# Performance work log

Hardware: AMD Instinct MI355X
Metric: run time of the kernel (lower is better)

Reference implementation:

```python
import jax, jax.numpy as jnp
import numpy as np

C, H_HEADS, L_LEV, M_PTS = 256, 4, 3, 4
TAU0 = 1.0


def _ln(x, g, b, eps=1e-5):
    mu = x.mean(-1, keepdims=True)
    var = ((x - mu) ** 2).mean(-1, keepdims=True)
    return (x - mu) * jax.lax.rsqrt(var + eps) * g + b


def _grid_sample(v, grid):
    """Bilinear grid_sample, padding_mode='zeros', align_corners=True.
    v: [B,C,Hin,Win], grid: [B,N,2] (x,y) in [-1,1] -> [B,N,C]"""
    B, Cc, Hin, Win = v.shape
    x = (grid[..., 0] + 1.0) * 0.5 * (Win - 1)
    y = (grid[..., 1] + 1.0) * 0.5 * (Hin - 1)
    x0 = jnp.floor(x); y0 = jnp.floor(y)
    wx1 = x - x0; wy1 = y - y0
    x0i = x0.astype(jnp.int32); y0i = y0.astype(jnp.int32)
    vflat = v.reshape(B, Cc, Hin * Win).transpose(0, 2, 1)  # [B,HW,C]

    def tap(yi, xi, w):
        valid = ((xi >= 0) & (xi < Win) & (yi >= 0) & (yi < Hin)).astype(v.dtype)
        idx = jnp.clip(yi, 0, Hin - 1) * Win + jnp.clip(xi, 0, Win - 1)  # [B,N]
        g = jax.vmap(lambda vf, i: vf[i])(vflat, idx)  # [B,N,C]
        return g * (w * valid)[..., None]

    return (tap(y0i, x0i, (1 - wy1) * (1 - wx1))
            + tap(y0i, x0i + 1, (1 - wy1) * wx1)
            + tap(y0i + 1, x0i, wy1 * (1 - wx1))
            + tap(y0i + 1, x0i + 1, wy1 * wx1))


def setup_inputs() -> dict:
    key = jax.random.key(0)
    ks = jax.random.split(key, 32)
    B, Hq, Wq = 2, 64, 64
    cins = [256, 512, 1024]
    d = {
        'S':  jax.random.normal(ks[0], (B, C, Hq, Wq), jnp.float32),
        'f0': jax.random.normal(ks[1], (B, cins[0], 64, 64), jnp.float32),
        'f1': jax.random.normal(ks[2], (B, cins[1], 32, 32), jnp.float32),
        'f2': jax.random.normal(ks[3], (B, cins[2], 16, 16), jnp.float32),
        'sim': jax.random.uniform(ks[4], (B, 1, Hq, Wq), jnp.float32),
        # 1x1 conv value projections per level
        'vw0': jax.random.normal(ks[5], (C, cins[0]), jnp.float32) * 0.02,
        'vb0': jnp.zeros((C,), jnp.float32),
        'vw1': jax.random.normal(ks[6], (C, cins[1]), jnp.float32) * 0.02,
        'vb1': jnp.zeros((C,), jnp.float32),
        'vw2': jax.random.normal(ks[7], (C, cins[2]), jnp.float32) * 0.02,
        'vb2': jnp.zeros((C,), jnp.float32),
        'q_w': jax.random.normal(ks[8], (C, C), jnp.float32) * 0.02,
        'q_b': jnp.zeros((C,), jnp.float32),
        # offset/weight predictors (non-zero so sampling is nontrivial)
        'off_w': jax.random.normal(ks[9], (H_HEADS * L_LEV * M_PTS * 2, C), jnp.float32) * 0.01,
        'off_b': jnp.zeros((H_HEADS * L_LEV * M_PTS * 2,), jnp.float32),
        'wgt_w': jax.random.normal(ks[10], (H_HEADS * L_LEV * M_PTS, C), jnp.float32) * 0.02,
        'wgt_b': jnp.zeros((H_HEADS * L_LEV * M_PTS,), jnp.float32),
        'out_w': jax.random.normal(ks[11], (C, H_HEADS * C), jnp.float32) * 0.02,
        'out_b': jnp.zeros((C,), jnp.float32),
        'lnq_g': jnp.ones((C,), jnp.float32), 'lnq_b': jnp.zeros((C,), jnp.float32),
        'lno_g': jnp.ones((C,), jnp.float32), 'lno_b': jnp.zeros((C,), jnp.float32),
        'fc1_w': jax.random.normal(ks[12], (4 * C, C), jnp.float32) * 0.02,
        'fc1_b': jnp.zeros((4 * C,), jnp.float32),
        'fc2_w': jax.random.normal(ks[13], (C, 4 * C), jnp.float32) * 0.02,
        'fc2_b': jnp.zeros((C,), jnp.float32),
    }
    return d


def reference(S, f0, f1, f2, sim, vw0, vb0, vw1, vb1, vw2, vb2, q_w, q_b,
              off_w, off_b, wgt_w, wgt_b, out_w, out_b,
              lnq_g, lnq_b, lno_g, lno_b, fc1_w, fc1_b, fc2_w, fc2_b):
    B, Cc, Hq, Wq = S.shape
    Nq = Hq * Wq
    S_seq = S.reshape(B, Cc, Nq).transpose(0, 2, 1)  # [B,Nq,C]
    Q = _ln(S_seq @ q_w.T + q_b, lnq_g, lnq_b)

    # reference points in [0,1], (x,y)
    ys = jnp.linspace(0.5 / Hq, 1 - 0.5 / Hq, Hq)
    xs = jnp.linspace(0.5 / Wq, 1 - 0.5 / Wq, Wq)
    yy, xx = jnp.meshgrid(ys, xs, indexing='ij')
    ref = jnp.stack([xx, yy], axis=-1).reshape(1, Nq, 2)

    feats = [(f0, vw0, vb0), (f1, vw1, vb1), (f2, vw2, vb2)]
    V = [jnp.einsum('bchw,oc->bohw', f, w) + b[None, :, None, None] for f, w, b in feats]

    off = (Q @ off_w.T + off_b).reshape(B, Nq, H_HEADS, L_LEV, M_PTS, 2)
    wts = (Q @ wgt_w.T + wgt_b).reshape(B, Nq, H_HEADS, L_LEV, M_PTS)

    sim2 = sim[:, 0].reshape(B, Nq, 1)
    tau = TAU0 / (sim2 + 0.001)
    wts = wts / tau.reshape(B, Nq, 1, 1, 1)
    wts = jax.nn.softmax(wts.reshape(B, Nq, H_HEADS, L_LEV * M_PTS), axis=-1)
    wts = wts.reshape(B, Nq, H_HEADS, L_LEV, M_PTS)

    acc = jnp.zeros((B, Nq, H_HEADS, Cc), S.dtype)
    for l in range(L_LEV):
        g01 = ref.reshape(1, Nq, 1, 1, 2) + off[:, :, :, l]  # [B,Nq,H,M,2]
        g = jnp.clip(jnp.tanh(g01 * 2.0 - 1.0), -1.0, 1.0)
        samp = _grid_sample(V[l], g.reshape(B, Nq * H_HEADS * M_PTS, 2))
        samp = samp.reshape(B, Nq, H_HEADS, M_PTS, Cc)
        acc = acc + jnp.einsum('bqhmc,bqhm->bqhc', samp, wts[:, :, :, l])

    Y = acc.reshape(B, Nq, H_HEADS * Cc) @ out_w.T + out_b
    Z = _ln(S_seq + Y, lno_g, lno_b)
    h = jax.nn.gelu(Z @ fc1_w.T + fc1_b, approximate=False)
    Z = Z + (h @ fc2_w.T + fc2_b)
    return Z.transpose(0, 2, 1).reshape(B, Cc, Hq, Wq)
```

## Files before the change

### kernel.cpp

```cpp
#include <hip/hip_runtime.h>
#include <hip/hip_bf16.h>
#include <math.h>

#define NQ 4096
#define CC 256

typedef __attribute__((ext_vector_type(8))) short bfrag;
typedef __attribute__((ext_vector_type(4))) float ffrag;

__device__ inline unsigned short f2bf(float x) {
  __hip_bfloat16 h = __float2bfloat16(x);
  return *reinterpret_cast<unsigned short*>(&h);
}

__device__ inline void gload16(const void* g, void* l) {
  __builtin_amdgcn_global_load_lds(
      (const __attribute__((address_space(1))) void*)g,
      (__attribute__((address_space(3))) void*)l, 16, 0, 0);
}

__device__ void tr64(const float* __restrict__ src,
                     unsigned short* __restrict__ dstb, int Cin, int P,
                     int p0, int c0, int b, float (*t)[73]) {
  int tid = threadIdx.x;
  int rx = tid & 15, ry = tid >> 4;
  const float* Sb = src + (size_t)b * Cin * P + p0 + rx * 4;
  #pragma unroll
  for (int i = 0; i < 4; i++) {
    int r = ry + i * 16;
    float4 v = *(const float4*)(Sb + (size_t)(c0 + r) * P);
    t[r][rx * 4 + 0] = v.x; t[r][rx * 4 + 1] = v.y;
    t[r][rx * 4 + 2] = v.z; t[r][rx * 4 + 3] = v.w;
  }
  __syncthreads();
  size_t ob = (size_t)b * P * Cin;
  #pragma unroll
  for (int i = 0; i < 4; i++) {
    int pr = ry + i * 16;
    float x0 = t[rx * 4 + 0][pr], x1 = t[rx * 4 + 1][pr];
    float x2 = t[rx * 4 + 2][pr], x3 = t[rx * 4 + 3][pr];
    size_t idx = ob + (size_t)(p0 + pr) * Cin + c0 + rx * 4;
    ushort4 u4;
    u4.x = f2bf(x0); u4.y = f2bf(x1); u4.z = f2bf(x2); u4.w = f2bf(x3);
    *(ushort4*)(dstb + idx) = u4;
  }
}

__global__ __launch_bounds__(256)
void prep_all_k(const float* S, const float* f0, const float* f1, const float* f2,
                const float* q_w, const float* off_w, const float* wgt_w,
                const float* vw0, const float* vw1, const float* vw2,
                const float* out_w, const float* fc1_w, const float* fc2_w,
                const float* off_b, const float* wgt_b,
                unsigned short* Sbf,
                unsigned short* Xf0, unsigned short* Xf1, unsigned short* Xf2,
                unsigned short* q_wb, unsigned short* owb,
                unsigned short* vw0b, unsigned short* vw1b, unsigned short* vw2b,
                unsigned short* out_wb, unsigned short* fc1_wb,
                unsigned short* fc2_wb, float* bias144) {
  __shared__ float t[64][73];
  int bid = blockIdx.x;
  if (bid < 512) {
    int l = bid;
    tr64(S, Sbf, 256, 4096, (l & 63) * 64, ((l >> 6) & 3) * 64, l >> 8, t);
  } else if (bid < 1024) {
    int l = bid - 512;
    tr64(f0, Xf0, 256, 4096, (l & 63) * 64, ((l >> 6) & 3) * 64, l >> 8, t);
  } else if (bid < 1280) {
    int l = bid - 1024;
    tr64(f1, Xf1, 512, 1024, (l & 15) * 64, ((l >> 4) & 7) * 64, l >> 7, t);
  } else if (bid < 1408) {
    int l = bid - 1280;
    tr64(f2, Xf2, 1024, 256, (l & 3) * 64, ((l >> 2) & 15) * 64, l >> 6, t);
  } else if (bid < 2688) {
    int i4 = (bid - 1408) * 256 + threadIdx.x;
    const float* src; unsigned short* dst;
    if (i4 < 16384)       { src = q_w;   dst = q_wb; }
    else if (i4 < 32768)  { i4 -= 16384;  src = vw0;   dst = vw0b; }
    else if (i4 < 65536)  { i4 -= 32768;  src = vw1;   dst = vw1b; }
    else if (i4 < 131072) { i4 -= 65536;  src = vw2;   dst = vw2b; }
    else if (i4 < 196608) { i4 -= 131072; src = out_w; dst = out_wb; }
    else if (i4 < 262144) { i4 -= 196608; src = fc1_w; dst = fc1_wb; }
    else                  { i4 -= 262144; src = fc2_w; dst = fc2_wb; }
    float4 v = ((const float4*)src)[i4];
    ushort4 u; u.x = f2bf(v.x); u.y = f2bf(v.y); u.z = f2bf(v.z); u.w = f2bf(v.w);
    ((ushort4*)dst)[i4] = u;
  } else {
    int e = (bid - 2688) * 256 + threadIdx.x;
    float v = (e < 24576) ? off_w[e] : (e < 36864 ? wgt_w[e - 24576] : 0.f);
    owb[e] = f2bf(v);
    if (e < 96) bias144[e] = off_b[e];
    else if (e < 144) bias144[e] = wgt_b[e - 96];
  }
}

template<int BM, int BN, int WM, int WN, int EPI>
__device__ __forceinline__ void gemm_body(
    const unsigned short* __restrict__ A, const unsigned short* __restrict__ B,
    const float* __restrict__ bias, float* __restrict__ outf,
    unsigned short* __restrict__ outb, int N, int K, int ldo,
    const float* __restrict__ Zres, float* __restrict__ outT,
    int m0, int n0, unsigned short* As, unsigned short* Bs) {
  constexpr int MI = BM / (WM * 16), NI = BN / (WN * 16);
  constexpr int TA = BM / 8, TB = BN / 8;
  constexpr int LBM = (BM == 32) ? 5 : (BM == 64) ? 6 : 7;
  constexpr int LBN = (BN == 64) ? 6 : (BN == 128) ? 7 : 8;
  int tid = threadIdx.x, wave = tid >> 6, lane = tid & 63;
  int quad = lane >> 4, l16 = lane & 15;
  int wm = wave / WN, wn = wave % WN;
  const int mbase = wm * (BM / WM), nbase = wn * (BN / WN);

  ffrag acc[MI][NI];
  #pragma unroll
  for (int i = 0; i < MI; i++)
    #pragma unroll
    for (int j = 0; j < NI; j++) acc[i][j] = (ffrag)0.f;

  for (int k0 = 0; k0 < K; k0 += 64) {
    __syncthreads();
    for (int t = wave; t < TA + TB; t += 4) {
      if (t < TA) {
        int s = t * 64 + lane;
        int kc = s >> LBM, r = s & (BM - 1);
        gload16(A + (size_t)(m0 + r) * K + k0 + kc * 8, (char*)As + t * 1024);
      } else {
        int s = (t - TA) * 64 + lane;
        int kc = s >> LBN, r = s & (BN - 1);
        gload16(B + (size_t)(n0 + r) * K + k0 + kc * 8, (char*)Bs + (t - TA) * 1024);
      }
    }
    __syncthreads();
    #pragma unroll
    for (int ks = 0; ks < 2; ks++) {
      bfrag af[MI], bf[NI];
      #pragma unroll
      for (int mi = 0; mi < MI; mi++)
        af[mi] = *(const bfrag*)(As + ((((ks * 4 + quad) << LBM) + mbase + mi * 16 + l16) << 3));
      #pragma unroll
      for (int ni = 0; ni < NI; ni++)
        bf[ni] = *(const bfrag*)(Bs + ((((ks * 4 + quad) << LBN) + nbase + ni * 16 + l16) << 3));
      #pragma unroll
      for (int mi = 0; mi < MI; mi++)
        #pragma unroll
        for (int ni = 0; ni < NI; ni++)
          acc[mi][ni] = __builtin_amdgcn_mfma_f32_16x16x32_bf16(
              af[mi], bf[ni], acc[mi][ni], 0, 0, 0);
    }
  }

  if (EPI == 2) {
    #pragma unroll
    for (int mi = 0; mi < MI; mi++) {
      int mrow = m0 + mbase + mi * 16 + quad * 4;
      int bb = mrow >> 12, q0 = mrow & (NQ - 1);
      #pragma unroll
      for (int ni = 0; ni < NI; ni++) {
        int n = n0 + nbase + ni * 16 + l16;
        float bv = bias[n];
        float4 v;
        v.x = acc[mi][ni][0] + bv + Zres[(size_t)(mrow + 0) * CC + n];
        v.y = acc[mi][ni][1] + bv + Zres[(size_t)(mrow + 1) * CC + n];
        v.z = acc[mi][ni][2] + bv + Zres[(size_t)(mrow + 2) * CC + n];
        v.w = acc[mi][ni][3] + bv + Zres[(size_t)(mrow + 3) * CC + n];
        *(float4*)(outT + ((size_t)(bb * CC + n)) * NQ + q0) = v;
      }
    }
  } else {
    #pragma unroll
    for (int mi = 0; mi < MI; mi++) {
      int mrow = m0 + mbase + mi * 16 + quad * 4;
      #pragma unroll
      for (int ni = 0; ni < NI; ni++) {
        int n = n0 + nbase + ni * 16 + l16;
        if (n < N) {
          float bv = bias[n];
          #pragma unroll
          for (int r = 0; r < 4; r++) {
            float v = acc[mi][ni][r] + bv;
            if (EPI == 1) {
              v = 0.5f * v * (1.f + erff(v * 0.70710678118654752f));
              outb[(size_t)(mrow + r) * ldo + n] = f2bf(v);
            } else if (EPI == 3) {
              outb[(size_t)(mrow + r) * ldo + n] = f2bf(v);
            } else {
              outf[(size_t)(mrow + r) * ldo + n] = v;
            }
          }
        }
      }
    }
  }
}

template<bool RES>
__device__ __forceinline__ void gemm_ln_body(
    const unsigned short* __restrict__ A, const unsigned short* __restrict__ B,
    const float* __restrict__ bias, const float* __restrict__ Sraw,
    float* __restrict__ outf, unsigned short* __restrict__ outb,
    const float* __restrict__ g, const float* __restrict__ be,
    int K, int m0, char* sm) {
  unsigned short* As = (unsigned short*)sm;
  unsigned short* Bs = (unsigned short*)(sm + 4096);
  float* L = (float*)sm;

  int tid = threadIdx.x, wave = tid >> 6, lane = tid & 63;
  int quad = lane >> 4, l16 = lane & 15;

  ffrag acc[2][4];
  #pragma unroll
  for (int i = 0; i < 2; i++)
    #pragma unroll
    for (int j = 0; j < 4; j++) acc[i][j] = (ffrag)0.f;

  for (int k0 = 0; k0 < K; k0 += 64) {
    __syncthreads();
    for (int t = wave; t < 36; t += 4) {
      if (t < 4) {
        int s = t * 64 + lane;
        int kc = s >> 5, r = s & 31;
        gload16(A + (size_t)(m0 + r) * K + k0 + kc * 8, sm + t * 1024);
      } else {
        int s = (t - 4) * 64 + lane;
        int kc = s >> 8, r = s & 255;
        gload16(B + (size_t)r * K + k0 + kc * 8, sm + 4096 + (t - 4) * 1024);
      }
    }
    __syncthreads();
    #pragma unroll
    for (int ks = 0; ks < 2; ks++) {
      bfrag af[2], bf[4];
      #pragma unroll
      for (int mi = 0; mi < 2; mi++)
        af[mi] = *(const bfrag*)(As + ((((ks * 4 + quad) << 5) + mi * 16 + l16) << 3));
      #pragma unroll
      for (int ni = 0; ni < 4; ni++)
        bf[ni] = *(const bfrag*)(Bs + ((((ks * 4 + quad) << 8) + wave * 64 + ni * 16 + l16) << 3));
      #pragma unroll
      for (int mi = 0; mi < 2; mi++)
        #pragma unroll
        for (int ni = 0; ni < 4; ni++)
          acc[mi][ni] = __builtin_amdgcn_mfma_f32_16x16x32_bf16(
              af[mi], bf[ni], acc[mi][ni], 0, 0, 0);
    }
  }
  __syncthreads();

  #pragma unroll
  for (int mi = 0; mi < 2; mi++) {
    int row = mi * 16 + quad * 4;
    int m = m0 + row;
    int bb = m >> 12, q0 = m & (NQ - 1);
    #pragma unroll
    for (int ni = 0; ni < 4; ni++) {
      int col = wave * 64 + ni * 16 + l16;
      float bv = bias[col];
      float4 s4 = make_float4(0.f, 0.f, 0.f, 0.f);
      if (RES) s4 = *(const float4*)(Sraw + ((size_t)(bb * CC + col)) * NQ + q0);
      L[(row + 0) * 264 + col] = acc[mi][ni][0] + bv + s4.x;
      L[(row + 1) * 264 + col] = acc[mi][ni][1] + bv + s4.y;
      L[(row + 2) * 264 + col] = acc[mi][ni][2] + bv + s4.z;
      L[(row + 3) * 264 + col] = acc[mi][ni][3] + bv + s4.w;
    }
  }
  __syncthreads();

  int row = tid >> 3, j = tid & 7;
  int seg = ((j + row) & 7) * 32;
  const float* Lr = L + row * 264 + seg;
  float s1 = 0.f, s2 = 0.f;
  #pragma unroll
  for (int i = 0; i < 8; i++) {
    float4 t4 = *(const float4*)(Lr + i * 4);
    s1 += t4.x + t4.y + t4.z + t4.w;
    s2 += t4.x * t4.x + t4.y * t4.y + t4.z * t4.z + t4.w * t4.w;
  }
  #pragma unroll
  for (int o = 1; o < 8; o <<= 1) {
    s1 += __shfl_xor(s1, o);
    s2 += __shfl_xor(s2, o);
  }
  float mu = s1 * (1.f / 256.f);
  float var = s2 * (1.f / 256.f) - mu * mu;
  float rs = rsqrtf(var + 1e-5f);
  int gm = m0 + row;
  #pragma unroll
  for (int i = 0; i < 8; i++) {
    int col = seg + i * 4;
    float4 t4 = *(const float4*)(Lr + i * 4);
    float4 gg = *(const float4*)(g + col);
    float4 bb4 = *(const float4*)(be + col);
    float4 y;
    y.x = (t4.x - mu) * rs * gg.x + bb4.x;
    y.y = (t4.y - mu) * rs * gg.y + bb4.y;
    y.z = (t4.z - mu) * rs * gg.z + bb4.z;
    y.w = (t4.w - mu) * rs * gg.w + bb4.w;
    ushort4 ub;
    ub.x = f2bf(y.x); ub.y = f2bf(y.y); ub.z = f2bf(y.z); ub.w = f2bf(y.w);
    *(ushort4*)(outb + (size_t)gm * CC + col) = ub;
    if (RES) *(float4*)(outf + (size_t)gm * CC + col) = y;
  }
}

__global__ __launch_bounds__(256)
void qv_k(const unsigned short* Sbf, const unsigned short* q_wb, const float* q_b,
          const float* lnq_g, const float* lnq_b, unsigned short* Qbf,
          const unsigned short* Xf0, const unsigned short* Xf1,
          const unsigned short* Xf2, const unsigned short* vw0b,
          const unsigned short* vw1b, const unsigned short* vw2b,
          const float* vb0, const float* vb1, const float* vb2,
          unsigned short* V0b, unsigned short* V1b, unsigned short* V2b) {
  __shared__ __attribute__((aligned(16))) char sm[36864];
  int bid = blockIdx.x;
  if (bid < 256) {
    gemm_ln_body<false>(Sbf, q_wb, q_b, nullptr, nullptr, Qbf,
                        lnq_g, lnq_b, 256, bid * 32, sm);
  } else {
    int lb = bid - 256;
    const unsigned short *A, *B; const float* bias; unsigned short* out; int K;
    if (lb < 256)      { A = Xf0; B = vw0b; bias = vb0; out = V0b; K = 256; }
    else if (lb < 320) { A = Xf1; B = vw1b; bias = vb1; out = V1b; K = 512;  lb -= 256; }
    else               { A = Xf2; B = vw2b; bias = vb2; out = V2b; K = 1024; lb -= 320; }
    int n0 = (lb & 1) * 128, m0 = (lb >> 1) * 64;
    gemm_body<64, 128, 2, 2, 3>(A, B, bias, nullptr, out, 256, K, 256,
                                nullptr, nullptr, m0, n0,
                                (unsigned short*)sm, (unsigned short*)(sm + 8192));
  }
}

__global__ __launch_bounds__(256)
void outln_k(const unsigned short* accbf, const unsigned short* out_wb,
             const float* out_b, const float* S, float* Z,
             unsigned short* Zbf, const float* lno_g, const float* lno_b) {
  __shared__ __attribute__((aligned(16))) char sm[36864];
  gemm_ln_body<true>(accbf, out_wb, out_b, S, Z, Zbf,
                     lno_g, lno_b, 1024, blockIdx.x * 32, sm);
}

__global__ __launch_bounds__(256)
void offwgt_k(const unsigned short* Qbf, const unsigned short* owb,
              const float* bias144, float* offwgt) {
  __shared__ __attribute__((aligned(16))) unsigned short As[4096];
  __shared__ __attribute__((aligned(16))) unsigned short Bs[8192];
  gemm_body<64, 128, 2, 2, 0>(Qbf, owb, bias144, offwgt, nullptr, 144, 256, 144,
                              nullptr, nullptr, blockIdx.y * 64, blockIdx.x * 128, As, Bs);
}

__global__ __launch_bounds__(256)
void fc1_k(const unsigned short* Zbf, const unsigned short* fc1_wb,
           const float* fc1_b, unsigned short* hbf) {
  __shared__ __attribute__((aligned(16))) unsigned short As[8192];
  __shared__ __attribute__((aligned(16))) unsigned short Bs[8192];
  gemm_body<128, 128, 2, 2, 1>(Zbf, fc1_wb, fc1_b, nullptr, hbf, 1024, 256, 1024,
                               nullptr, nullptr, blockIdx.y * 128, blockIdx.x * 128, As, Bs);
}

__global__ __launch_bounds__(256)
void fc2_k(const unsigned short* hbf, const unsigned short* fc2_wb,
           const float* fc2_b, const float* Z, float* outp) {
  __shared__ __attribute__((aligned(16))) unsigned short As[4096];
  __shared__ __attribute__((aligned(16))) unsigned short Bs[4096];
  gemm_body<64, 64, 2, 2, 2>(hbf, fc2_wb, fc2_b, nullptr, nullptr, 256, 1024, 256,
                             Z, outp, blockIdx.y * 64, blockIdx.x * 64, As, Bs);
}

__global__ __launch_bounds__(256)
void sample_k(const float* __restrict__ ow, const float* __restrict__ sim,
              const unsigned short* __restrict__ V0, const unsigned short* __restrict__ V1,
              const unsigned short* __restrict__ V2, unsigned short* __restrict__ acc) {
  int bn = blockIdx.x;
  int q = ((bn & 7) << 10) | (bn >> 3);
  int b = q >> 12, n = q & (NQ - 1);
  int tid = threadIdx.x, head = tid >> 6, lane = tid & 63;
  int half = lane >> 5, l32 = lane & 31;

  __shared__ float s_w[48];
  __shared__ int   s_xy[48][2];
  __shared__ float s_f[48][2];
  __shared__ uint2 s_ow[192];

  if (tid < 48) {
    int hh = tid / 12, pt = tid % 12, l = pt >> 2, mm = pt & 3;
    int oidx = (hh * 3 + l) * 4 + mm;
    float offx = ow[(size_t)q * 144 + oidx * 2 + 0];
    float offy = ow[(size_t)q * 144 + oidx * 2 + 1];
    float refx = ((n & 63) + 0.5f) * (1.f / 64.f);
    float refy = ((n >> 6) + 0.5f) * (1.f / 64.f);
    float gx = tanhf((refx + offx) * 2.f - 1.f);
    float gy = tanhf((refy + offy) * 2.f - 1.f);
    gx = fminf(1.f, fmaxf(-1.f, gx));
    gy = fminf(1.f, fmaxf(-1.f, gy));
    int Wl = 64 >> l;
    float x = (gx + 1.f) * 0.5f * (float)(Wl - 1);
    float y = (gy + 1.f) * 0.5f * (float)(Wl - 1);
    float x0 = floorf(x), y0 = floorf(y);
    s_xy[tid][0] = (int)x0;
    s_xy[tid][1] = (int)y0;
    s_f[tid][0] = x - x0;
    s_f[tid][1] = y - y0;
    s_w[tid] = ow[(size_t)q * 144 + 96 + oidx] * (sim[q] + 0.001f);
  }
  __syncthreads();
  if (tid < 4) {
    float mx = -1e30f;
    #pragma unroll
    for (int i = 0; i < 12; i++) mx = fmaxf(mx, s_w[tid * 12 + i]);
    float e[12], ssum = 0.f;
    #pragma unroll
    for (int i = 0; i < 12; i++) { e[i] = expf(s_w[tid * 12 + i] - mx); ssum += e[i]; }
    float inv = 1.f / ssum;
    #pragma unroll
    for (int i = 0; i < 12; i++) s_w[tid * 12 + i] = e[i] * inv;
  }
  __syncthreads();
  if (tid < 192) {
    int s = tid >> 2, tap = tid & 3;
    int l = (s % 12) >> 2;
    int Wl = 64 >> l;
    int X = s_xy[s][0] + (tap & 1), Y = s_xy[s][1] + (tap >> 1);
    bool valid = (X >= 0 && X < Wl && Y >= 0 && Y < Wl);
    float wx = (tap & 1) ? s_f[s][0] : 1.f - s_f[s][0];
    float wy = (tap >> 1) ? s_f[s][1] : 1.f - s_f[s][1];
    float twt = valid ? s_w[s] * wx * wy : 0.f;
    int Xc = min(max(X, 0), Wl - 1), Yc = min(max(Y, 0), Wl - 1);
    s_ow[tid].x = (unsigned)((Yc * Wl + Xc) << 8);
    s_ow[tid].y = __float_as_uint(twt);
  }
  __syncthreads();

  const unsigned short* B0 = V0 + (size_t)b * 4096 * CC;
  const unsigned short* B1 = V1 + (size_t)b * 1024 * CC;
  const unsigned short* B2 = V2 + (size_t)b * 256 * CC;
  int ch8 = l32 * 8;
  float a0 = 0.f, a1 = 0.f, a2 = 0.f, a3 = 0.f;
  float a4 = 0.f, a5 = 0.f, a6 = 0.f, a7 = 0.f;
  #pragma unroll
  for (int it = 0; it < 24; it++) {
    const unsigned short* base = (it < 8) ? B0 : (it < 16) ? B1 : B2;
    uint2 owv = s_ow[head * 48 + it * 2 + half];
    float w = __uint_as_float(owv.y);
    const uint4 u = *(const uint4*)(base + owv.x + ch8);
    a0 = fmaf(w, __uint_as_float(u.x << 16), a0);
    a1 = fmaf(w, __uint_as_float(u.x & 0xffff0000u), a1);
    a2 = fmaf(w, __uint_as_float(u.y << 16), a2);
    a3 = fmaf(w, __uint_as_float(u.y & 0xffff0000u), a3);
    a4 = fmaf(w, __uint_as_float(u.z << 16), a4);
    a5 = fmaf(w, __uint_as_float(u.z & 0xffff0000u), a5);
    a6 = fmaf(w, __uint_as_float(u.w << 16), a6);
    a7 = fmaf(w, __uint_as_float(u.w & 0xffff0000u), a7);
  }
  a0 += __shfl_xor(a0, 32); a1 += __shfl_xor(a1, 32);
  a2 += __shfl_xor(a2, 32); a3 += __shfl_xor(a3, 32);
  a4 += __shfl_xor(a4, 32); a5 += __shfl_xor(a5, 32);
  a6 += __shfl_xor(a6, 32); a7 += __shfl_xor(a7, 32);
  if (half == 0) {
    uint4 r;
    r.x = (unsigned)f2bf(a0) | ((unsigned)f2bf(a1) << 16);
    r.y = (unsigned)f2bf(a2) | ((unsigned)f2bf(a3) << 16);
    r.z = (unsigned)f2bf(a4) | ((unsigned)f2bf(a5) << 16);
    r.w = (unsigned)f2bf(a6) | ((unsigned)f2bf(a7) << 16);
    *(uint4*)(acc + (size_t)q * 1024 + head * CC + ch8) = r;
  }
}

extern "C" void kernel_launch(void* const* d_in, const int* in_sizes, int n_in,
                              void* d_out, int out_size, void* d_ws, size_t ws_size,
                              hipStream_t stream) {
  const float* S     = (const float*)d_in[0];
  const float* f0    = (const float*)d_in[1];
  const float* f1    = (const float*)d_in[2];
  const float* f2    = (const float*)d_in[3];
  const float* sim   = (const float*)d_in[4];
  const float* vw0   = (const float*)d_in[5];
  const float* vb0   = (const float*)d_in[6];
  const float* vw1   = (const float*)d_in[7];
  const float* vb1   = (const float*)d_in[8];
  const float* vw2   = (const float*)d_in[9];
  const float* vb2   = (const float*)d_in[10];
  const float* q_w   = (const float*)d_in[11];
  const float* q_b   = (const float*)d_in[12];
  const float* off_w = (const float*)d_in[13];
  const float* off_b = (const float*)d_in[14];
  const float* wgt_w = (const float*)d_in[15];
  const float* wgt_b = (const float*)d_in[16];
  const float* out_w = (const float*)d_in[17];
  const float* out_b = (const float*)d_in[18];
  const float* lnq_g = (const float*)d_in[19];
  const float* lnq_b = (const float*)d_in[20];
  const float* lno_g = (const float*)d_in[21];
  const float* lno_b = (const float*)d_in[22];
  const float* fc1_w = (const float*)d_in[23];
  const float* fc1_b = (const float*)d_in[24];
  const float* fc2_w = (const float*)d_in[25];
  const float* fc2_b = (const float*)d_in[26];

  char* p = (char*)d_ws;
  float* Z      = (float*)p; p += 8388608;
  float* offwgt = (float*)p; p += 4718592;
  float* bias144 = (float*)p; p += 1024;
  unsigned short* Sbf   = (unsigned short*)p; p += 4194304;
  unsigned short* Qbf   = (unsigned short*)p; p += 4194304;
  unsigned short* accbf = (unsigned short*)p; p += 16777216;
  unsigned short* V0b   = (unsigned short*)p; p += 4194304;
  unsigned short* V1b   = (unsigned short*)p; p += 1048576;
  unsigned short* V2b   = (unsigned short*)p; p += 262144;
  unsigned short* q_wb   = (unsigned short*)p; p += 131072;
  unsigned short* owb    = (unsigned short*)p; p += 131072;
  unsigned short* vw0b   = (unsigned short*)p; p += 131072;
  unsigned short* vw1b   = (unsigned short*)p; p += 262144;
  unsigned short* vw2b   = (unsigned short*)p; p += 524288;
  unsigned short* out_wb = (unsigned short*)p; p += 524288;
  unsigned short* fc1_wb = (unsigned short*)p; p += 524288;
  unsigned short* fc2_wb = (unsigned short*)p; p += 524288;

  unsigned short* Xf0 = accbf;
  unsigned short* Xf1 = accbf + 2097152;
  unsigned short* Xf2 = accbf + 3145728;
  unsigned short* Zbf = Qbf;
  unsigned short* hbf = accbf;
  float* outp = (float*)d_out;

  prep_all_k<<<2944, 256, 0, stream>>>(S, f0, f1, f2, q_w, off_w, wgt_w,
      vw0, vw1, vw2, out_w, fc1_w, fc2_w, off_b, wgt_b,
      Sbf, Xf0, Xf1, Xf2, q_wb, owb, vw0b, vw1b, vw2b, out_wb,
      fc1_wb, fc2_wb, bias144);

  qv_k<<<592, 256, 0, stream>>>(Sbf, q_wb, q_b, lnq_g, lnq_b, Qbf,
      Xf0, Xf1, Xf2, vw0b, vw1b, vw2b, vb0, vb1, vb2, V0b, V1b, V2b);

  offwgt_k<<<dim3(2, 128), 256, 0, stream>>>(Qbf, owb, bias144, offwgt);

  sample_k<<<8192, 256, 0, stream>>>(offwgt, sim, V0b, V1b, V2b, accbf);

  outln_k<<<256, 256, 0, stream>>>(accbf, out_wb, out_b, S, Z, Zbf,
      lno_g, lno_b);

  fc1_k<<<dim3(8, 64), 256, 0, stream>>>(Zbf, fc1_wb, fc1_b, hbf);

  fc2_k<<<dim3(4, 128), 256, 0, stream>>>(hbf, fc2_wb, fc2_b, Z, outp);
}
```

Measured before the change: 276.3 us.

## Split-K the long-K GEMMs with separate reduction and epilogue kernels

The out-projection, fc2 and the level-1/2 value projections are split along K into 4 (or 2) partial GEMMs that write fp32 partials. Separate kernels then sum the partials and apply bias, residual, LayerNorm or the transpose to the output layout. The offset GEMM is merged with the V1/V2 reductions into one launch, and fc1 uses smaller tiles. The aim is more blocks per GEMM so the GPU fills better, at the cost of extra fp32 partial traffic through memory and two more launches.

Result: slower. 286.5 us (+3.7%).

```diff
diff --git a/kernel.cpp b/kernel.cpp
--- a/kernel.cpp
+++ b/kernel.cpp
@@ -98,9 +98,8 @@
 __device__ __forceinline__ void gemm_body(
     const unsigned short* __restrict__ A, const unsigned short* __restrict__ B,
     const float* __restrict__ bias, float* __restrict__ outf,
-    unsigned short* __restrict__ outb, int N, int K, int ldo,
-    const float* __restrict__ Zres, float* __restrict__ outT,
-    int m0, int n0, unsigned short* As, unsigned short* Bs) {
+    unsigned short* __restrict__ outb, int N, int Kloop, int lda, int ldb,
+    int ldo, int m0, int n0, unsigned short* As, unsigned short* Bs) {
   constexpr int MI = BM / (WM * 16), NI = BN / (WN * 16);
   constexpr int TA = BM / 8, TB = BN / 8;
   constexpr int LBM = (BM == 32) ? 5 : (BM == 64) ? 6 : 7;
@@ -116,17 +115,17 @@
     #pragma unroll
     for (int j = 0; j < NI; j++) acc[i][j] = (ffrag)0.f;
 
-  for (int k0 = 0; k0 < K; k0 += 64) {
+  for (int k0 = 0; k0 < Kloop; k0 += 64) {
     __syncthreads();
     for (int t = wave; t < TA + TB; t += 4) {
       if (t < TA) {
         int s = t * 64 + lane;
         int kc = s >> LBM, r = s & (BM - 1);
-        gload16(A + (size_t)(m0 + r) * K + k0 + kc * 8, (char*)As + t * 1024);
+        gload16(A + (size_t)(m0 + r) * lda + k0 + kc * 8, (char*)As + t * 1024);
       } else {
         int s = (t - TA) * 64 + lane;
         int kc = s >> LBN, r = s & (BN - 1);
-        gload16(B + (size_t)(n0 + r) * K + k0 + kc * 8, (char*)Bs + (t - TA) * 1024);
+        gload16(B + (size_t)(n0 + r) * ldb + k0 + kc * 8, (char*)Bs + (t - TA) * 1024);
       }
     }
     __syncthreads();
@@ -148,43 +147,24 @@
     }
   }
 
-  if (EPI == 2) {
-    #pragma unroll
-    for (int mi = 0; mi < MI; mi++) {
-      int mrow = m0 + mbase + mi * 16 + quad * 4;
-      int bb = mrow >> 12, q0 = mrow & (NQ - 1);
-      #pragma unroll
-      for (int ni = 0; ni < NI; ni++) {
-        int n = n0 + nbase + ni * 16 + l16;
-        float bv = bias[n];
-        float4 v;
-        v.x = acc[mi][ni][0] + bv + Zres[(size_t)(mrow + 0) * CC + n];
-        v.y = acc[mi][ni][1] + bv + Zres[(size_t)(mrow + 1) * CC + n];
-        v.z = acc[mi][ni][2] + bv + Zres[(size_t)(mrow + 2) * CC + n];
-        v.w = acc[mi][ni][3] + bv + Zres[(size_t)(mrow + 3) * CC + n];
-        *(float4*)(outT + ((size_t)(bb * CC + n)) * NQ + q0) = v;
-      }
-    }
-  } else {
-    #pragma unroll
-    for (int mi = 0; mi < MI; mi++) {
-      int mrow = m0 + mbase + mi * 16 + quad * 4;
-      #pragma unroll
-      for (int ni = 0; ni < NI; ni++) {
-        int n = n0 + nbase + ni * 16 + l16;
-        if (n < N) {
-          float bv = bias[n];
-          #pragma unroll
-          for (int r = 0; r < 4; r++) {
-            float v = acc[mi][ni][r] + bv;
-            if (EPI == 1) {
-              v = 0.5f * v * (1.f + erff(v * 0.70710678118654752f));
-              outb[(size_t)(mrow + r) * ldo + n] = f2bf(v);
-            } else if (EPI == 3) {
-              outb[(size_t)(mrow + r) * ldo + n] = f2bf(v);
-            } else {
-              outf[(size_t)(mrow + r) * ldo + n] = v;
-            }
+  #pragma unroll
+  for (int mi = 0; mi < MI; mi++) {
+    int mrow = m0 + mbase + mi * 16 + quad * 4;
+    #pragma unroll
+    for (int ni = 0; ni < NI; ni++) {
+      int n = n0 + nbase + ni * 16 + l16;
+      if (n < N) {
+        float bv = (EPI == 4) ? 0.f : bias[n];
+        #pragma unroll
+        for (int r = 0; r < 4; r++) {
+          float v = acc[mi][ni][r] + bv;
+          if (EPI == 1) {
+            v = 0.5f * v * (1.f + erff(v * 0.70710678118654752f));
+            outb[(size_t)(mrow + r) * ldo + n] = f2bf(v);
+          } else if (EPI == 3) {
+            outb[(size_t)(mrow + r) * ldo + n] = f2bf(v);
+          } else {
+            outf[(size_t)(mrow + r) * ldo + n] = v;
           }
         }
       }
@@ -192,16 +172,15 @@
   }
 }
 
-template<bool RES>
-__device__ __forceinline__ void gemm_ln_body(
+__device__ __forceinline__ void gemm_ln_q(
     const unsigned short* __restrict__ A, const unsigned short* __restrict__ B,
-    const float* __restrict__ bias, const float* __restrict__ Sraw,
-    float* __restrict__ outf, unsigned short* __restrict__ outb,
+    const float* __restrict__ bias, unsigned short* __restrict__ outb,
     const float* __restrict__ g, const float* __restrict__ be,
-    int K, int m0, char* sm) {
+    int m0, char* sm) {
   unsigned short* As = (unsigned short*)sm;
   unsigned short* Bs = (unsigned short*)(sm + 4096);
   float* L = (float*)sm;
+  const int K = 256;
 
   int tid = threadIdx.x, wave = tid >> 6, lane = tid & 63;
   int quad = lane >> 4, l16 = lane & 15;
@@ -248,18 +227,13 @@
   #pragma unroll
   for (int mi = 0; mi < 2; mi++) {
     int row = mi * 16 + quad * 4;
-    int m = m0 + row;
-    int bb = m >> 12, q0 = m & (NQ - 1);
     #pragma unroll
     for (int ni = 0; ni < 4; ni++) {
       int col = wave * 64 + ni * 16 + l16;
       float bv = bias[col];
-      float4 s4 = make_float4(0.f, 0.f, 0.f, 0.f);
-      if (RES) s4 = *(const float4*)(Sraw + ((size_t)(bb * CC + col)) * NQ + q0);
-      L[(row + 0) * 264 + col] = acc[mi][ni][0] + bv + s4.x;
-      L[(row + 1) * 264 + col] = acc[mi][ni][1] + bv + s4.y;
-      L[(row + 2) * 264 + col] = acc[mi][ni][2] + bv + s4.z;
-      L[(row + 3) * 264 + col] = acc[mi][ni][3] + bv + s4.w;
+      #pragma unroll
+      for (int r = 0; r < 4; r++)
+        L[(row + r) * 264 + col] = acc[mi][ni][r] + bv;
     }
   }
   __syncthreads();
@@ -286,6 +260,145 @@
   #pragma unroll
   for (int i = 0; i < 8; i++) {
     int col = seg + i * 4;
+    float4 t4 = *(const float4*)(Lr + i * 4);
+    float4 gg = *(const float4*)(g + col);
+    float4 bb4 = *(const float4*)(be + col);
+    ushort4 ub;
+    ub.x = f2bf((t4.x - mu) * rs * gg.x + bb4.x);
+    ub.y = f2bf((t4.y - mu) * rs * gg.y + bb4.y);
+    ub.z = f2bf((t4.z - mu) * rs * gg.z + bb4.z);
+    ub.w = f2bf((t4.w - mu) * rs * gg.w + bb4.w);
+    *(ushort4*)(outb + (size_t)gm * CC + col) = ub;
+  }
+}
+
+__global__ __launch_bounds__(256)
+void qv_k(const unsigned short* Sbf, const unsigned short* q_wb, const float* q_b,
+          const float* lnq_g, const float* lnq_b, unsigned short* Qbf,
+          const unsigned short* Xf0, const unsigned short* Xf1,
+          const unsigned short* Xf2, const unsigned short* vw0b,
+          const unsigned short* vw1b, const unsigned short* vw2b,
+          const float* vb0, unsigned short* V0b, float* Vp1, float* Vp2) {
+  __shared__ __attribute__((aligned(16))) char sm[36864];
+  int bid = blockIdx.x;
+  unsigned short* As = (unsigned short*)sm;
+  unsigned short* Bs = (unsigned short*)(sm + 8192);
+  if (bid < 256) {
+    gemm_ln_q(Sbf, q_wb, q_b, Qbf, lnq_g, lnq_b, bid * 32, sm);
+  } else if (bid < 512) {
+    int t = bid - 256;
+    gemm_body<64, 128, 2, 2, 3>(Xf0, vw0b, vb0, nullptr, V0b, 256, 256, 256, 256,
+                                256, (t >> 1) * 64, (t & 1) * 128, As, Bs);
+  } else if (bid < 640) {
+    int l = bid - 512, ks = l >> 6, t = l & 63;
+    gemm_body<64, 128, 2, 2, 4>(Xf1 + ks * 256, vw1b + ks * 256, nullptr,
+                                Vp1 + (size_t)ks * 524288, nullptr, 256, 256, 512, 512,
+                                256, (t >> 1) * 64, (t & 1) * 128, As, Bs);
+  } else {
+    int l = bid - 640, ks = l >> 4, t = l & 15;
+    gemm_body<64, 128, 2, 2, 4>(Xf2 + ks * 256, vw2b + ks * 256, nullptr,
+                                Vp2 + (size_t)ks * 131072, nullptr, 256, 256, 1024, 1024,
+                                256, (t >> 1) * 64, (t & 1) * 128, As, Bs);
+  }
+}
+
+__global__ __launch_bounds__(256)
+void offv_k(const unsigned short* Qbf, const unsigned short* owb,
+            const float* bias144, float* offwgt,
+            const float* Vp1, const float* Vp2, const float* vb1,
+            const float* vb2, unsigned short* V1b, unsigned short* V2b) {
+  __shared__ __attribute__((aligned(16))) unsigned short As[4096];
+  __shared__ __attribute__((aligned(16))) unsigned short Bs[8192];
+  int bid = blockIdx.x;
+  if (bid < 256) {
+    gemm_body<64, 128, 2, 2, 0>(Qbf, owb, bias144, offwgt, nullptr, 144, 256, 256,
+                                256, 144, (bid >> 1) * 64, (bid & 1) * 128, As, Bs);
+  } else if (bid < 768) {
+    int e4 = (bid - 256) * 256 + threadIdx.x;
+    const float4* P = (const float4*)Vp1;
+    float4 a = P[e4], b = P[e4 + 131072];
+    float4 bb = *(const float4*)(vb1 + ((e4 << 2) & 255));
+    ushort4 u;
+    u.x = f2bf(a.x + b.x + bb.x); u.y = f2bf(a.y + b.y + bb.y);
+    u.z = f2bf(a.z + b.z + bb.z); u.w = f2bf(a.w + b.w + bb.w);
+    ((ushort4*)V1b)[e4] = u;
+  } else {
+    int e4 = (bid - 768) * 256 + threadIdx.x;
+    const float4* P = (const float4*)Vp2;
+    float4 a = P[e4], b = P[e4 + 32768], c = P[e4 + 65536], d = P[e4 + 98304];
+    float4 bb = *(const float4*)(vb2 + ((e4 << 2) & 255));
+    ushort4 u;
+    u.x = f2bf(a.x + b.x + c.x + d.x + bb.x);
+    u.y = f2bf(a.y + b.y + c.y + d.y + bb.y);
+    u.z = f2bf(a.z + b.z + c.z + d.z + bb.z);
+    u.w = f2bf(a.w + b.w + c.w + d.w + bb.w);
+    ((ushort4*)V2b)[e4] = u;
+  }
+}
+
+__global__ __launch_bounds__(256)
+void outA_k(const unsigned short* accbf, const unsigned short* out_wb, float* Op) {
+  __shared__ __attribute__((aligned(16))) char sm[36864];
+  int ks = blockIdx.y;
+  gemm_body<32, 256, 1, 4, 4>(accbf + ks * 256, out_wb + ks * 256, nullptr,
+                              Op + (size_t)ks * 2097152, nullptr, 256, 256, 1024,
+                              1024, 256, blockIdx.x * 32, 0,
+                              (unsigned short*)sm, (unsigned short*)(sm + 4096));
+}
+
+__global__ __launch_bounds__(256)
+void outB_k(const float* __restrict__ Op, const float* __restrict__ S,
+            const float* __restrict__ out_b, const float* __restrict__ g,
+            const float* __restrict__ be, float* __restrict__ Zf,
+            unsigned short* __restrict__ Zbf) {
+  __shared__ float Ls[16][264];
+  int q0 = blockIdx.x * 16;
+  int b = q0 >> 12, qq = q0 & (NQ - 1);
+  int t = threadIdx.x;
+  {
+    int cs = t >> 2, j = (t & 3) * 4;
+    #pragma unroll
+    for (int c0 = 0; c0 < 256; c0 += 64) {
+      float4 sv = *(const float4*)(S + (((size_t)(b * 256 + c0 + cs)) << 12) + qq + j);
+      Ls[j + 0][c0 + cs] = sv.x; Ls[j + 1][c0 + cs] = sv.y;
+      Ls[j + 2][c0 + cs] = sv.z; Ls[j + 3][c0 + cs] = sv.w;
+    }
+  }
+  __syncthreads();
+  int c = t;
+  float bv = out_b[c];
+  float val[16];
+  #pragma unroll
+  for (int r = 0; r < 16; r++) {
+    size_t idx = (size_t)(q0 + r) * 256 + c;
+    val[r] = Op[idx] + Op[idx + 2097152] + Op[idx + 4194304] + Op[idx + 6291456]
+           + bv + Ls[r][c];
+  }
+  __syncthreads();
+  #pragma unroll
+  for (int r = 0; r < 16; r++) Ls[r][c] = val[r];
+  __syncthreads();
+  int row = t >> 4, lg = t & 15;
+  const float* Lr = &Ls[row][lg * 16];
+  float s1 = 0.f, s2 = 0.f;
+  #pragma unroll
+  for (int i = 0; i < 4; i++) {
+    float4 t4 = *(const float4*)(Lr + i * 4);
+    s1 += t4.x + t4.y + t4.z + t4.w;
+    s2 += t4.x * t4.x + t4.y * t4.y + t4.z * t4.z + t4.w * t4.w;
+  }
+  #pragma unroll
+  for (int o = 1; o < 16; o <<= 1) {
+    s1 += __shfl_xor(s1, o);
+    s2 += __shfl_xor(s2, o);
+  }
+  float mu = s1 * (1.f / 256.f);
+  float var = s2 * (1.f / 256.f) - mu * mu;
+  float rs = rsqrtf(var + 1e-5f);
+  int gm = q0 + row;
+  #pragma unroll
+  for (int i = 0; i < 4; i++) {
+    int col = lg * 16 + i * 4;
     float4 t4 = *(const float4*)(Lr + i * 4);
     float4 gg = *(const float4*)(g + col);
     float4 bb4 = *(const float4*)(be + col);
@@ -294,73 +407,52 @@
     y.y = (t4.y - mu) * rs * gg.y + bb4.y;
     y.z = (t4.z - mu) * rs * gg.z + bb4.z;
     y.w = (t4.w - mu) * rs * gg.w + bb4.w;
+    *(float4*)(Zf + (size_t)gm * CC + col) = y;
     ushort4 ub;
     ub.x = f2bf(y.x); ub.y = f2bf(y.y); ub.z = f2bf(y.z); ub.w = f2bf(y.w);
-    *(ushort4*)(outb + (size_t)gm * CC + col) = ub;
-    if (RES) *(float4*)(outf + (size_t)gm * CC + col) = y;
-  }
-}
-
-__global__ __launch_bounds__(256)
-void qv_k(const unsigned short* Sbf, const unsigned short* q_wb, const float* q_b,
-          const float* lnq_g, const float* lnq_b, unsigned short* Qbf,
-          const unsigned short* Xf0, const unsigned short* Xf1,
-          const unsigned short* Xf2, const unsigned short* vw0b,
-          const unsigned short* vw1b, const unsigned short* vw2b,
-          const float* vb0, const float* vb1, const float* vb2,
-          unsigned short* V0b, unsigned short* V1b, unsigned short* V2b) {
-  __shared__ __attribute__((aligned(16))) char sm[36864];
-  int bid = blockIdx.x;
-  if (bid < 256) {
-    gemm_ln_body<false>(Sbf, q_wb, q_b, nullptr, nullptr, Qbf,
-                        lnq_g, lnq_b, 256, bid * 32, sm);
-  } else {
-    int lb = bid - 256;
-    const unsigned short *A, *B; const float* bias; unsigned short* out; int K;
-    if (lb < 256)      { A = Xf0; B = vw0b; bias = vb0; out = V0b; K = 256; }
-    else if (lb < 320) { A = Xf1; B = vw1b; bias = vb1; out = V1b; K = 512;  lb -= 256; }
-    else               { A = Xf2; B = vw2b; bias = vb2; out = V2b; K = 1024; lb -= 320; }
-    int n0 = (lb & 1) * 128, m0 = (lb >> 1) * 64;
-    gemm_body<64, 128, 2, 2, 3>(A, B, bias, nullptr, out, 256, K, 256,
-                                nullptr, nullptr, m0, n0,
-                                (unsigned short*)sm, (unsigned short*)(sm + 8192));
-  }
-}
-
-__global__ __launch_bounds__(256)
-void outln_k(const unsigned short* accbf, const unsigned short* out_wb,
-             const float* out_b, const float* S, float* Z,
-             unsigned short* Zbf, const float* lno_g, const float* lno_b) {
-  __shared__ __attribute__((aligned(16))) char sm[36864];
-  gemm_ln_body<true>(accbf, out_wb, out_b, S, Z, Zbf,
-                     lno_g, lno_b, 1024, blockIdx.x * 32, sm);
-}
-
-__global__ __launch_bounds__(256)
-void offwgt_k(const unsigned short* Qbf, const unsigned short* owb,
-              const float* bias144, float* offwgt) {
+    *(ushort4*)(Zbf + (size_t)gm * CC + col) = ub;
+  }
+}
+
+__global__ __launch_bounds__(256)
+void fc1_k(const unsigned short* Zbf, const unsigned short* fc1_wb,
+           const float* fc1_b, unsigned short* hbf) {
   __shared__ __attribute__((aligned(16))) unsigned short As[4096];
   __shared__ __attribute__((aligned(16))) unsigned short Bs[8192];
-  gemm_body<64, 128, 2, 2, 0>(Qbf, owb, bias144, offwgt, nullptr, 144, 256, 144,
-                              nullptr, nullptr, blockIdx.y * 64, blockIdx.x * 128, As, Bs);
-}
-
-__global__ __launch_bounds__(256)
-void fc1_k(const unsigned short* Zbf, const unsigned short* fc1_wb,
-           const float* fc1_b, unsigned short* hbf) {
-  __shared__ __attribute__((aligned(16))) unsigned short As[8192];
-  __shared__ __attribute__((aligned(16))) unsigned short Bs[8192];
-  gemm_body<128, 128, 2, 2, 1>(Zbf, fc1_wb, fc1_b, nullptr, hbf, 1024, 256, 1024,
-                               nullptr, nullptr, blockIdx.y * 128, blockIdx.x * 128, As, Bs);
-}
-
-__global__ __launch_bounds__(256)
-void fc2_k(const unsigned short* hbf, const unsigned short* fc2_wb,
-           const float* fc2_b, const float* Z, float* outp) {
-  __shared__ __attribute__((aligned(16))) unsigned short As[4096];
-  __shared__ __attribute__((aligned(16))) unsigned short Bs[4096];
-  gemm_body<64, 64, 2, 2, 2>(hbf, fc2_wb, fc2_b, nullptr, nullptr, 256, 1024, 256,
-                             Z, outp, blockIdx.y * 64, blockIdx.x * 64, As, Bs);
+  gemm_body<64, 128, 2, 2, 1>(Zbf, fc1_wb, fc1_b, nullptr, hbf, 1024, 256, 256,
+                              256, 1024, blockIdx.y * 64, blockIdx.x * 128, As, Bs);
+}
+
+__global__ __launch_bounds__(256)
+void fc2A_k(const unsigned short* hbf, const unsigned short* fc2_wb, float* Fp) {
+  __shared__ __attribute__((aligned(16))) char sm[36864];
+  int ks = blockIdx.y;
+  gemm_body<32, 256, 1, 4, 4>(hbf + ks * 256, fc2_wb + ks * 256, nullptr,
+                              Fp + (size_t)ks * 2097152, nullptr, 256, 256, 1024,
+                              1024, 256, blockIdx.x * 32, 0,
+                              (unsigned short*)sm, (unsigned short*)(sm + 4096));
+}
+
+__global__ __launch_bounds__(256)
+void fc2B_k(const float* __restrict__ Fp, const float* __restrict__ Z,
+            const float* __restrict__ fc2_b, float* __restrict__ outp) {
+  int q0 = blockIdx.x * 64;
+  int b = q0 >> 12, qq = q0 & (NQ - 1);
+  int n = threadIdx.x;
+  float bv = fc2_b[n];
+  float* od = outp + (((size_t)(b * 256 + n)) << 12) + qq;
+  #pragma unroll
+  for (int g4 = 0; g4 < 16; g4++) {
+    float4 o;
+    #pragma unroll
+    for (int j = 0; j < 4; j++) {
+      size_t idx = (size_t)(q0 + g4 * 4 + j) * 256 + n;
+      float v = Fp[idx] + Fp[idx + 2097152] + Fp[idx + 4194304] + Fp[idx + 6291456]
+              + Z[idx] + bv;
+      ((float*)&o)[j] = v;
+    }
+    *(float4*)(od + g4 * 4) = o;
+  }
 }
 
 __global__ __launch_bounds__(256)
@@ -497,6 +589,9 @@
   float* Z      = (float*)p; p += 8388608;
   float* offwgt = (float*)p; p += 4718592;
   float* bias144 = (float*)p; p += 1024;
+  float* Pp     = (float*)p; p += 33554432;
+  float* Vp1    = (float*)p; p += 4194304;
+  float* Vp2    = (float*)p; p += 2097152;
   unsigned short* Sbf   = (unsigned short*)p; p += 4194304;
   unsigned short* Qbf   = (unsigned short*)p; p += 4194304;
   unsigned short* accbf = (unsigned short*)p; p += 16777216;
@@ -524,17 +619,21 @@
       Sbf, Xf0, Xf1, Xf2, q_wb, owb, vw0b, vw1b, vw2b, out_wb,
       fc1_wb, fc2_wb, bias144);
 
-  qv_k<<<592, 256, 0, stream>>>(Sbf, q_wb, q_b, lnq_g, lnq_b, Qbf,
-      Xf0, Xf1, Xf2, vw0b, vw1b, vw2b, vb0, vb1, vb2, V0b, V1b, V2b);
-
-  offwgt_k<<<dim3(2, 128), 256, 0, stream>>>(Qbf, owb, bias144, offwgt);
+  qv_k<<<704, 256, 0, stream>>>(Sbf, q_wb, q_b, lnq_g, lnq_b, Qbf,
+      Xf0, Xf1, Xf2, vw0b, vw1b, vw2b, vb0, V0b, Vp1, Vp2);
+
+  offv_k<<<896, 256, 0, stream>>>(Qbf, owb, bias144, offwgt,
+      Vp1, Vp2, vb1, vb2, V1b, V2b);
 
   sample_k<<<8192, 256, 0, stream>>>(offwgt, sim, V0b, V1b, V2b, accbf);
 
-  outln_k<<<256, 256, 0, stream>>>(accbf, out_wb, out_b, S, Z, Zbf,
-      lno_g, lno_b);
-
-  fc1_k<<<dim3(8, 64), 256, 0, stream>>>(Zbf, fc1_wb, fc1_b, hbf);
-
-  fc2_k<<<dim3(4, 128), 256, 0, stream>>>(hbf, fc2_wb, fc2_b, Z, outp);
-}
+  outA_k<<<dim3(256, 4), 256, 0, stream>>>(accbf, out_wb, Pp);
+
+  outB_k<<<512, 256, 0, stream>>>(Pp, S, out_b, lno_g, lno_b, Z, Zbf);
+
+  fc1_k<<<dim3(8, 128), 256, 0, stream>>>(Zbf, fc1_wb, fc1_b, hbf);
+
+  fc2A_k<<<dim3(256, 4), 256, 0, stream>>>(hbf, fc2_wb, Pp);
+
+  fc2B_k<<<128, 256, 0, stream>>>(Pp, Z, fc2_b, outp);
+}
```
